# Performance work log

Hardware: AMD Instinct MI355X
Metric: run time of the kernel (lower is better)

Reference implementation:

```python
import jax, jax.numpy as jnp
import numpy as np

NEG_INF = -1e15  # matches masked_fill value -1000000000000000.0
ALPHA = 0.2      # leakyReLU negative slope


def setup_inputs() -> dict:
    key = jax.random.key(0)
    k1, k2, k3, k4 = jax.random.split(key, 4)
    N, F_IN, F_OUT = 8192, 256, 64
    x = jax.random.normal(k1, (N, F_IN), dtype=jnp.float32)
    mask = jax.random.randint(k2, (N, N), 0, 2, dtype=jnp.int32)
    trans = jax.random.normal(k3, (F_IN, F_OUT), dtype=jnp.float32) * 0.1
    attn = jax.random.normal(k4, (2 * F_OUT, 1), dtype=jnp.float32) * 0.1
    return {"x": x, "mask": mask, "trans": trans, "attn": attn}


def reference(x, mask, trans, attn):
    d = trans.shape[1]
    h = x @ trans                                  # [N, d]
    e1 = h @ attn[:d, :]                           # [N, 1]
    e2 = h @ attn[d:, :]                           # [N, 1]
    scores = jax.nn.leaky_relu(e1 + e2.T, negative_slope=ALPHA)  # [N, N]
    masked = jnp.where(mask == 0, NEG_INF, scores)
    attention = jax.nn.softmax(masked, axis=1)
    return attention @ h                           # [N, d]
```

## Files before the change

### kernel.cpp

```cpp
#include <hip/hip_runtime.h>
#include <hip/hip_bf16.h>
#include <math.h>

#define N 8192
#define FIN 256
#define D 64
#define ALPHA 0.2f

typedef __attribute__((ext_vector_type(8))) short bf16x8;
typedef __attribute__((ext_vector_type(4))) float f32x4;

__global__ __launch_bounds__(256) void k_h_e(
    const float* __restrict__ x, const float* __restrict__ trans,
    const float* __restrict__ attn,
    __hip_bfloat16* __restrict__ hF, float* __restrict__ e1, float* __restrict__ e2)
{
    __shared__ float xs[8 * FIN];
    __shared__ __hip_bfloat16 hl[8 * D];
    const int t = threadIdx.x;
    const int r0 = blockIdx.x * 8;

    #pragma unroll
    for (int v = 0; v < 2; ++v) {
        int idx = t + 256 * v;
        ((float4*)xs)[idx] = ((const float4*)(x + (size_t)r0 * FIN))[idx];
    }
    __syncthreads();

    const int lane = t & 63, w = t >> 6;
    const float* xa = xs + (2 * w) * FIN;
    const float* xb = xs + (2 * w + 1) * FIN;
    float acca = 0.f, accb = 0.f;
    #pragma unroll 8
    for (int k = 0; k < FIN; ++k) {
        const float tv = trans[k * D + lane];
        acca = fmaf(xa[k], tv, acca);
        accb = fmaf(xb[k], tv, accb);
    }
    const int ra = r0 + 2 * w, rb = ra + 1;

    const float a1 = attn[lane], a2 = attn[D + lane];
    float p1a = acca * a1, p2a = acca * a2;
    float p1b = accb * a1, p2b = accb * a2;
    #pragma unroll
    for (int mm = 1; mm <= 32; mm <<= 1) {
        p1a += __shfl_xor(p1a, mm);
        p2a += __shfl_xor(p2a, mm);
        p1b += __shfl_xor(p1b, mm);
        p2b += __shfl_xor(p2b, mm);
    }
    if (lane == 0) { e1[ra] = p1a; e2[ra] = p2a; e1[rb] = p1b; e2[rb] = p2b; }

    hl[(2 * w) * D + lane]     = __float2bfloat16(acca);
    hl[(2 * w + 1) * D + lane] = __float2bfloat16(accb);
    __syncthreads();
    if (t < D) {
        const int q = t >> 4, m = t & 15;
        const int cb = r0 >> 5, jgrp = (r0 >> 3) & 3;
        union { bf16x8 v; __hip_bfloat16 h[8]; } o;
        #pragma unroll
        for (int r = 0; r < 8; ++r) o.h[r] = hl[r * D + q * 16 + m];
        *(bf16x8*)(hF + (((size_t)cb * 4 + q) * 64 + jgrp * 16 + m) * 8) = o.v;
    }
}

__global__ __launch_bounds__(256) void k_attn(
    const int* __restrict__ mask, const __hip_bfloat16* __restrict__ hF,
    const float* __restrict__ e1, const float* __restrict__ e2,
    float* __restrict__ acc_part, float* __restrict__ l_part, int cs)
{
    const int t = threadIdx.x;
    const int lane = t & 63, wave = t >> 6;
    const int i0 = (blockIdx.y * 4 + wave) * 16;
    const int sp = blockIdx.x;
    const int c0 = sp * cs;
    const int m = lane & 15, quad = lane >> 4;
    const int row = i0 + m;
    const float er = e1[row];
    const size_t mrow = (size_t)row * N;

    const __hip_bfloat16* hfp = hF + (((size_t)(c0 >> 5)) * 4 * 64 + lane) * 8;

    f32x4 acc0 = {0.f, 0.f, 0.f, 0.f};
    f32x4 acc1 = {0.f, 0.f, 0.f, 0.f};
    f32x4 acc2 = {0.f, 0.f, 0.f, 0.f};
    f32x4 acc3 = {0.f, 0.f, 0.f, 0.f};
    float lsum = 0.f;

    const int iters = cs >> 5;
    #pragma unroll 2
    for (int it = 0; it < iters; ++it) {
        const int jb = c0 + it * 32 + quad * 8;
        const int4   m0 = *(const int4*)(mask + mrow + jb);
        const int4   m1 = *(const int4*)(mask + mrow + jb + 4);
        const float4 ea = *(const float4*)(e2 + jb);
        const float4 eb = *(const float4*)(e2 + jb + 4);
        const bf16x8* hq = (const bf16x8*)(hfp + (size_t)it * 2048);
        const bf16x8 b0 = hq[0];
        const bf16x8 b1 = hq[64];
        const bf16x8 b2 = hq[128];
        const bf16x8 b3 = hq[192];

        float s0 = er + ea.x; s0 = s0 > 0.f ? s0 : ALPHA * s0;
        float s1 = er + ea.y; s1 = s1 > 0.f ? s1 : ALPHA * s1;
        float s2 = er + ea.z; s2 = s2 > 0.f ? s2 : ALPHA * s2;
        float s3 = er + ea.w; s3 = s3 > 0.f ? s3 : ALPHA * s3;
        float s4 = er + eb.x; s4 = s4 > 0.f ? s4 : ALPHA * s4;
        float s5 = er + eb.y; s5 = s5 > 0.f ? s5 : ALPHA * s5;
        float s6 = er + eb.z; s6 = s6 > 0.f ? s6 : ALPHA * s6;
        float s7 = er + eb.w; s7 = s7 > 0.f ? s7 : ALPHA * s7;
        const float p0 = m0.x ? __expf(s0) : 0.f;
        const float p1 = m0.y ? __expf(s1) : 0.f;
        const float p2 = m0.z ? __expf(s2) : 0.f;
        const float p3 = m0.w ? __expf(s3) : 0.f;
        const float p4 = m1.x ? __expf(s4) : 0.f;
        const float p5 = m1.y ? __expf(s5) : 0.f;
        const float p6 = m1.z ? __expf(s6) : 0.f;
        const float p7 = m1.w ? __expf(s7) : 0.f;

        union { bf16x8 v; __hip_bfloat162 h2[4]; } af;
        af.h2[0] = __float22bfloat162_rn(make_float2(p0, p1));
        af.h2[1] = __float22bfloat162_rn(make_float2(p2, p3));
        af.h2[2] = __float22bfloat162_rn(make_float2(p4, p5));
        af.h2[3] = __float22bfloat162_rn(make_float2(p6, p7));

        lsum += ((p0 + p1) + (p2 + p3)) + ((p4 + p5) + (p6 + p7));

        acc0 = __builtin_amdgcn_mfma_f32_16x16x32_bf16(af.v, b0, acc0, 0, 0, 0);
        acc1 = __builtin_amdgcn_mfma_f32_16x16x32_bf16(af.v, b1, acc1, 0, 0, 0);
        acc2 = __builtin_amdgcn_mfma_f32_16x16x32_bf16(af.v, b2, acc2, 0, 0, 0);
        acc3 = __builtin_amdgcn_mfma_f32_16x16x32_bf16(af.v, b3, acc3, 0, 0, 0);
    }

    lsum += __shfl_xor(lsum, 16);
    lsum += __shfl_xor(lsum, 32);
    if (quad == 0) l_part[(size_t)sp * N + row] = lsum;

    #pragma unroll
    for (int reg = 0; reg < 4; ++reg) {
        const size_t rbase = ((size_t)sp * N + i0 + quad * 4 + reg) * D;
        acc_part[rbase + m     ] = acc0[reg];
        acc_part[rbase + m + 16] = acc1[reg];
        acc_part[rbase + m + 32] = acc2[reg];
        acc_part[rbase + m + 48] = acc3[reg];
    }
}

__global__ __launch_bounds__(256) void k_reduce(
    const float* __restrict__ acc_part, const float* __restrict__ l_part,
    float* __restrict__ out, int nsplit)
{
    const int idx = blockIdx.x * 256 + threadIdx.x;
    const int row = idx >> 6;
    float sum = 0.f, l = 0.f;
    for (int s = 0; s < nsplit; ++s) {
        sum += acc_part[(size_t)s * N * D + idx];
        l   += l_part[(size_t)s * N + row];
    }
    out[idx] = sum / l;
}

extern "C" void kernel_launch(void* const* d_in, const int* in_sizes, int n_in,
                              void* d_out, int out_size, void* d_ws, size_t ws_size,
                              hipStream_t stream) {
    const float* x     = (const float*)d_in[0];
    const int*   mask  = (const int*)d_in[1];
    const float* trans = (const float*)d_in[2];
    const float* attn  = (const float*)d_in[3];
    float* out = (float*)d_out;

    char* ws = (char*)d_ws;
    __hip_bfloat16* hF = (__hip_bfloat16*)ws;
    char* p = ws + (size_t)D * N * sizeof(__hip_bfloat16);
    float* e1 = (float*)p;            p += (size_t)N * sizeof(float);
    float* e2 = (float*)p;            p += (size_t)N * sizeof(float);

    const size_t used = (size_t)(p - ws);
    int nsplit = 4;
    while (nsplit > 1) {
        size_t need = used + (size_t)nsplit * N * sizeof(float)
                    + (size_t)nsplit * N * D * sizeof(float);
        if (need <= ws_size) break;
        nsplit >>= 1;
    }
    float* l_part = (float*)p;
    float* acc_part = l_part + (size_t)nsplit * N;

    k_h_e<<<N / 8, 256, 0, stream>>>(x, trans, attn, hF, e1, e2);
    dim3 g2(nsplit, N / 64);
    k_attn<<<g2, 256, 0, stream>>>(mask, hF, e1, e2, acc_part, l_part, N / nsplit);
    k_reduce<<<(N * D) / 256, 256, 0, stream>>>(acc_part, l_part, out, nsplit);
}
```

Measured before the change: 427.9 us.

## Stage mask rows into LDS via coalesced global_load_lds and prefetch h/e2 operands

The attention kernel now copies each wave's 16 mask rows, 256 columns at a time, into a padded per-wave LDS buffer using async global_load_lds. Each lane issues fully coalesced 16-byte loads instead of strided per-row loads. The h fragments and e2 values are software-prefetched one step ahead within each 256-column chunk. The intent is better DRAM efficiency on the 256MB mask stream. The cost is about 66KB of LDS per block, which may reduce occupancy, and a full vmcnt wait that serializes load and compute per chunk.

```diff
diff --git a/kernel.cpp b/kernel.cpp
--- a/kernel.cpp
+++ b/kernel.cpp
@@ -6,6 +6,8 @@
 #define FIN 256
 #define D 64
 #define ALPHA 0.2f
+#define SROW 1040
+#define WBUF (16 * SROW)
 
 typedef __attribute__((ext_vector_type(8))) short bf16x8;
 typedef __attribute__((ext_vector_type(4))) float f32x4;
@@ -69,6 +71,7 @@
     const float* __restrict__ e1, const float* __restrict__ e2,
     float* __restrict__ acc_part, float* __restrict__ l_part, int cs)
 {
+    __shared__ __align__(16) char smem[4 * WBUF];
     const int t = threadIdx.x;
     const int lane = t & 63, wave = t >> 6;
     const int i0 = (blockIdx.y * 4 + wave) * 16;
@@ -77,8 +80,9 @@
     const int m = lane & 15, quad = lane >> 4;
     const int row = i0 + m;
     const float er = e1[row];
-    const size_t mrow = (size_t)row * N;
-
+
+    char* sw = smem + wave * WBUF;
+    const char* swm = sw + m * SROW;
     const __hip_bfloat16* hfp = hF + (((size_t)(c0 >> 5)) * 4 * 64 + lane) * 8;
 
     f32x4 acc0 = {0.f, 0.f, 0.f, 0.f};
@@ -87,49 +91,79 @@
     f32x4 acc3 = {0.f, 0.f, 0.f, 0.f};
     float lsum = 0.f;
 
-    const int iters = cs >> 5;
-    #pragma unroll 2
-    for (int it = 0; it < iters; ++it) {
-        const int jb = c0 + it * 32 + quad * 8;
-        const int4   m0 = *(const int4*)(mask + mrow + jb);
-        const int4   m1 = *(const int4*)(mask + mrow + jb + 4);
-        const float4 ea = *(const float4*)(e2 + jb);
-        const float4 eb = *(const float4*)(e2 + jb + 4);
-        const bf16x8* hq = (const bf16x8*)(hfp + (size_t)it * 2048);
-        const bf16x8 b0 = hq[0];
-        const bf16x8 b1 = hq[64];
-        const bf16x8 b2 = hq[128];
-        const bf16x8 b3 = hq[192];
-
-        float s0 = er + ea.x; s0 = s0 > 0.f ? s0 : ALPHA * s0;
-        float s1 = er + ea.y; s1 = s1 > 0.f ? s1 : ALPHA * s1;
-        float s2 = er + ea.z; s2 = s2 > 0.f ? s2 : ALPHA * s2;
-        float s3 = er + ea.w; s3 = s3 > 0.f ? s3 : ALPHA * s3;
-        float s4 = er + eb.x; s4 = s4 > 0.f ? s4 : ALPHA * s4;
-        float s5 = er + eb.y; s5 = s5 > 0.f ? s5 : ALPHA * s5;
-        float s6 = er + eb.z; s6 = s6 > 0.f ? s6 : ALPHA * s6;
-        float s7 = er + eb.w; s7 = s7 > 0.f ? s7 : ALPHA * s7;
-        const float p0 = m0.x ? __expf(s0) : 0.f;
-        const float p1 = m0.y ? __expf(s1) : 0.f;
-        const float p2 = m0.z ? __expf(s2) : 0.f;
-        const float p3 = m0.w ? __expf(s3) : 0.f;
-        const float p4 = m1.x ? __expf(s4) : 0.f;
-        const float p5 = m1.y ? __expf(s5) : 0.f;
-        const float p6 = m1.z ? __expf(s6) : 0.f;
-        const float p7 = m1.w ? __expf(s7) : 0.f;
-
-        union { bf16x8 v; __hip_bfloat162 h2[4]; } af;
-        af.h2[0] = __float22bfloat162_rn(make_float2(p0, p1));
-        af.h2[1] = __float22bfloat162_rn(make_float2(p2, p3));
-        af.h2[2] = __float22bfloat162_rn(make_float2(p4, p5));
-        af.h2[3] = __float22bfloat162_rn(make_float2(p6, p7));
-
-        lsum += ((p0 + p1) + (p2 + p3)) + ((p4 + p5) + (p6 + p7));
-
-        acc0 = __builtin_amdgcn_mfma_f32_16x16x32_bf16(af.v, b0, acc0, 0, 0, 0);
-        acc1 = __builtin_amdgcn_mfma_f32_16x16x32_bf16(af.v, b1, acc1, 0, 0, 0);
-        acc2 = __builtin_amdgcn_mfma_f32_16x16x32_bf16(af.v, b2, acc2, 0, 0, 0);
-        acc3 = __builtin_amdgcn_mfma_f32_16x16x32_bf16(af.v, b3, acc3, 0, 0, 0);
+    const int nss = cs >> 8;
+
+    for (int ss = 0; ss < nss; ++ss) {
+        const int cb0 = c0 + ss * 256;
+        #pragma unroll
+        for (int r = 0; r < 16; ++r) {
+            const int* g = mask + (size_t)(i0 + r) * N + cb0 + lane * 4;
+            char* l = sw + r * SROW + lane * 16;
+            __builtin_amdgcn_global_load_lds(
+                (const __attribute__((address_space(1))) void*)g,
+                (__attribute__((address_space(3))) void*)l, 16, 0, 0);
+        }
+        __builtin_amdgcn_s_waitcnt(0x0F70);
+
+        const int itg0 = ss * 8;
+        bf16x8 pb0, pb1, pb2, pb3; float4 pea, peb;
+        {
+            const size_t ito = (size_t)itg0 * 2048;
+            pb0 = *(const bf16x8*)(hfp + ito);
+            pb1 = *(const bf16x8*)(hfp + ito + 512);
+            pb2 = *(const bf16x8*)(hfp + ito + 1024);
+            pb3 = *(const bf16x8*)(hfp + ito + 1536);
+            const int jb = cb0 + quad * 8;
+            pea = *(const float4*)(e2 + jb);
+            peb = *(const float4*)(e2 + jb + 4);
+        }
+        #pragma unroll
+        for (int p = 0; p < 8; ++p) {
+            const bf16x8 b0 = pb0, b1 = pb1, b2 = pb2, b3 = pb3;
+            const float4 ea = pea, eb = peb;
+            if (p < 7) {
+                const size_t ito = (size_t)(itg0 + p + 1) * 2048;
+                pb0 = *(const bf16x8*)(hfp + ito);
+                pb1 = *(const bf16x8*)(hfp + ito + 512);
+                pb2 = *(const bf16x8*)(hfp + ito + 1024);
+                pb3 = *(const bf16x8*)(hfp + ito + 1536);
+                const int jb = cb0 + (p + 1) * 32 + quad * 8;
+                pea = *(const float4*)(e2 + jb);
+                peb = *(const float4*)(e2 + jb + 4);
+            }
+            const int4 m0 = *(const int4*)(swm + p * 128 + quad * 32);
+            const int4 m1 = *(const int4*)(swm + p * 128 + quad * 32 + 16);
+
+            float s0 = er + ea.x; s0 = s0 > 0.f ? s0 : ALPHA * s0;
+            float s1 = er + ea.y; s1 = s1 > 0.f ? s1 : ALPHA * s1;
+            float s2 = er + ea.z; s2 = s2 > 0.f ? s2 : ALPHA * s2;
+            float s3 = er + ea.w; s3 = s3 > 0.f ? s3 : ALPHA * s3;
+            float s4 = er + eb.x; s4 = s4 > 0.f ? s4 : ALPHA * s4;
+            float s5 = er + eb.y; s5 = s5 > 0.f ? s5 : ALPHA * s5;
+            float s6 = er + eb.z; s6 = s6 > 0.f ? s6 : ALPHA * s6;
+            float s7 = er + eb.w; s7 = s7 > 0.f ? s7 : ALPHA * s7;
+            const float p0 = m0.x ? __expf(s0) : 0.f;
+            const float p1 = m0.y ? __expf(s1) : 0.f;
+            const float p2 = m0.z ? __expf(s2) : 0.f;
+            const float p3 = m0.w ? __expf(s3) : 0.f;
+            const float p4 = m1.x ? __expf(s4) : 0.f;
+            const float p5 = m1.y ? __expf(s5) : 0.f;
+            const float p6 = m1.z ? __expf(s6) : 0.f;
+            const float p7 = m1.w ? __expf(s7) : 0.f;
+
+            union { bf16x8 v; __hip_bfloat162 h2[4]; } af;
+            af.h2[0] = __float22bfloat162_rn(make_float2(p0, p1));
+            af.h2[1] = __float22bfloat162_rn(make_float2(p2, p3));
+            af.h2[2] = __float22bfloat162_rn(make_float2(p4, p5));
+            af.h2[3] = __float22bfloat162_rn(make_float2(p6, p7));
+
+            lsum += ((p0 + p1) + (p2 + p3)) + ((p4 + p5) + (p6 + p7));
+
+            acc0 = __builtin_amdgcn_mfma_f32_16x16x32_bf16(af.v, b0, acc0, 0, 0, 0);
+            acc1 = __builtin_amdgcn_mfma_f32_16x16x32_bf16(af.v, b1, acc1, 0, 0, 0);
+            acc2 = __builtin_amdgcn_mfma_f32_16x16x32_bf16(af.v, b2, acc2, 0, 0, 0);
+            acc3 = __builtin_amdgcn_mfma_f32_16x16x32_bf16(af.v, b3, acc3, 0, 0, 0);
+        }
     }
 
     lsum += __shfl_xor(lsum, 16);
```

Result: faster. 391.9 us (-8.4%).

## Double-buffer mask tiles into LDS via global_load_lds and prefetch h fragments

Applied to the files above, without the earlier changes.

Rewrites the attention kernel's main loop as a software pipeline. Each wave stages 16x128 mask tiles into padded LDS buffers with asynchronous global_load_lds and register-prefetches the next stage's bf16 h fragments while computing the current stage. The e2 slice is staged once into shared memory. The split count is fixed at 8 with 1024-column chunks, and launch bounds now request 2 blocks per CU. This is meant to hide the latency of the 256MB mask stream, at the cost of a large LDS footprint, many extra registers for the prefetched fragments, more partial sums for the reduce pass, and hand-coded waitcnt values that may be fragile.

```diff
diff --git a/kernel.cpp b/kernel.cpp
--- a/kernel.cpp
+++ b/kernel.cpp
@@ -6,6 +6,11 @@
 #define FIN 256
 #define D 64
 #define ALPHA 0.2f
+#define NSPLIT 8
+#define CS 1024
+#define NSS 8
+#define SROW 528
+#define WBUF (16 * SROW)
 
 typedef __attribute__((ext_vector_type(8))) short bf16x8;
 typedef __attribute__((ext_vector_type(4))) float f32x4;
@@ -64,21 +69,92 @@
     }
 }
 
-__global__ __launch_bounds__(256) void k_attn(
+
+#define GLDS(G, L, SZ) __builtin_amdgcn_global_load_lds( \
+    (const __attribute__((address_space(1))) void*)(G),  \
+    (__attribute__((address_space(3))) void*)(L), (SZ), 0, 0)
+
+#define STAGE_MASK(SSV, BUF)                                           \
+    {                                                                  \
+        const int cb_ = c0 + (SSV) * 128;                              \
+        _Pragma("unroll")                                              \
+        for (int r_ = 0; r_ < 16; ++r_) {                              \
+            const int* g_ = mask + (size_t)(i0 + r_) * N + cb_ + lane; \
+            char* l_ = (BUF) + r_ * SROW + lane * 4;                   \
+            GLDS(g_, l_, 4);                                           \
+            GLDS(g_ + 64, l_ + 256, 4);                                \
+        }                                                              \
+    }
+
+#define HOIST_HF(SSV, HX)                                              \
+    {                                                                  \
+        _Pragma("unroll")                                              \
+        for (int p_ = 0; p_ < 4; ++p_) {                               \
+            const size_t ito_ = (size_t)((SSV) * 4 + p_) * 2048;       \
+            HX[4 * p_ + 0] = *(const bf16x8*)(hfp + ito_);             \
+            HX[4 * p_ + 1] = *(const bf16x8*)(hfp + ito_ + 512);       \
+            HX[4 * p_ + 2] = *(const bf16x8*)(hfp + ito_ + 1024);      \
+            HX[4 * p_ + 3] = *(const bf16x8*)(hfp + ito_ + 1536);      \
+        }                                                              \
+    }
+
+#define COMPUTE_SS(SSV, BUF, HX)                                               \
+    {                                                                          \
+        const char* swm_ = (BUF) + m * SROW;                                   \
+        _Pragma("unroll")                                                      \
+        for (int p_ = 0; p_ < 4; ++p_) {                                       \
+            const int4 m0 = *(const int4*)(swm_ + p_ * 128 + quad * 32);       \
+            const int4 m1 = *(const int4*)(swm_ + p_ * 128 + quad * 32 + 16);  \
+            const int ec_ = (SSV) * 128 + p_ * 32 + quad * 8;                  \
+            const float4 ea = *(const float4*)(se2 + ec_);                     \
+            const float4 eb = *(const float4*)(se2 + ec_ + 4);                 \
+            float s0 = er + ea.x; s0 = s0 > 0.f ? s0 : ALPHA * s0;             \
+            float s1 = er + ea.y; s1 = s1 > 0.f ? s1 : ALPHA * s1;             \
+            float s2 = er + ea.z; s2 = s2 > 0.f ? s2 : ALPHA * s2;             \
+            float s3 = er + ea.w; s3 = s3 > 0.f ? s3 : ALPHA * s3;             \
+            float s4 = er + eb.x; s4 = s4 > 0.f ? s4 : ALPHA * s4;             \
+            float s5 = er + eb.y; s5 = s5 > 0.f ? s5 : ALPHA * s5;             \
+            float s6 = er + eb.z; s6 = s6 > 0.f ? s6 : ALPHA * s6;             \
+            float s7 = er + eb.w; s7 = s7 > 0.f ? s7 : ALPHA * s7;             \
+            const float p0 = m0.x ? __expf(s0) : 0.f;                          \
+            const float p1 = m0.y ? __expf(s1) : 0.f;                          \
+            const float p2 = m0.z ? __expf(s2) : 0.f;                          \
+            const float p3 = m0.w ? __expf(s3) : 0.f;                          \
+            const float p4 = m1.x ? __expf(s4) : 0.f;                          \
+            const float p5 = m1.y ? __expf(s5) : 0.f;                          \
+            const float p6 = m1.z ? __expf(s6) : 0.f;                          \
+            const float p7 = m1.w ? __expf(s7) : 0.f;                          \
+            union { bf16x8 v; __hip_bfloat162 h2[4]; } af;                     \
+            af.h2[0] = __float22bfloat162_rn(make_float2(p0, p1));             \
+            af.h2[1] = __float22bfloat162_rn(make_float2(p2, p3));             \
+            af.h2[2] = __float22bfloat162_rn(make_float2(p4, p5));             \
+            af.h2[3] = __float22bfloat162_rn(make_float2(p6, p7));             \
+            lsum += ((p0 + p1) + (p2 + p3)) + ((p4 + p5) + (p6 + p7));         \
+            acc0 = __builtin_amdgcn_mfma_f32_16x16x32_bf16(af.v, HX[4*p_+0], acc0, 0, 0, 0); \
+            acc1 = __builtin_amdgcn_mfma_f32_16x16x32_bf16(af.v, HX[4*p_+1], acc1, 0, 0, 0); \
+            acc2 = __builtin_amdgcn_mfma_f32_16x16x32_bf16(af.v, HX[4*p_+2], acc2, 0, 0, 0); \
+            acc3 = __builtin_amdgcn_mfma_f32_16x16x32_bf16(af.v, HX[4*p_+3], acc3, 0, 0, 0); \
+        }                                                                      \
+    }
+
+__global__ __launch_bounds__(256, 2) void k_attn(
     const int* __restrict__ mask, const __hip_bfloat16* __restrict__ hF,
     const float* __restrict__ e1, const float* __restrict__ e2,
-    float* __restrict__ acc_part, float* __restrict__ l_part, int cs)
+    float* __restrict__ acc_part, float* __restrict__ l_part)
 {
+    __shared__ __align__(16) char smask[8 * WBUF];
+    __shared__ __align__(16) float se2[CS];
     const int t = threadIdx.x;
     const int lane = t & 63, wave = t >> 6;
     const int i0 = (blockIdx.y * 4 + wave) * 16;
     const int sp = blockIdx.x;
-    const int c0 = sp * cs;
+    const int c0 = sp * CS;
     const int m = lane & 15, quad = lane >> 4;
     const int row = i0 + m;
     const float er = e1[row];
-    const size_t mrow = (size_t)row * N;
-
+
+    char* bufA = smask + (wave * 2 + 0) * WBUF;
+    char* bufB = smask + (wave * 2 + 1) * WBUF;
     const __hip_bfloat16* hfp = hF + (((size_t)(c0 >> 5)) * 4 * 64 + lane) * 8;
 
     f32x4 acc0 = {0.f, 0.f, 0.f, 0.f};
@@ -86,51 +162,31 @@
     f32x4 acc2 = {0.f, 0.f, 0.f, 0.f};
     f32x4 acc3 = {0.f, 0.f, 0.f, 0.f};
     float lsum = 0.f;
-
-    const int iters = cs >> 5;
-    #pragma unroll 2
-    for (int it = 0; it < iters; ++it) {
-        const int jb = c0 + it * 32 + quad * 8;
-        const int4   m0 = *(const int4*)(mask + mrow + jb);
-        const int4   m1 = *(const int4*)(mask + mrow + jb + 4);
-        const float4 ea = *(const float4*)(e2 + jb);
-        const float4 eb = *(const float4*)(e2 + jb + 4);
-        const bf16x8* hq = (const bf16x8*)(hfp + (size_t)it * 2048);
-        const bf16x8 b0 = hq[0];
-        const bf16x8 b1 = hq[64];
-        const bf16x8 b2 = hq[128];
-        const bf16x8 b3 = hq[192];
-
-        float s0 = er + ea.x; s0 = s0 > 0.f ? s0 : ALPHA * s0;
-        float s1 = er + ea.y; s1 = s1 > 0.f ? s1 : ALPHA * s1;
-        float s2 = er + ea.z; s2 = s2 > 0.f ? s2 : ALPHA * s2;
-        float s3 = er + ea.w; s3 = s3 > 0.f ? s3 : ALPHA * s3;
-        float s4 = er + eb.x; s4 = s4 > 0.f ? s4 : ALPHA * s4;
-        float s5 = er + eb.y; s5 = s5 > 0.f ? s5 : ALPHA * s5;
-        float s6 = er + eb.z; s6 = s6 > 0.f ? s6 : ALPHA * s6;
-        float s7 = er + eb.w; s7 = s7 > 0.f ? s7 : ALPHA * s7;
-        const float p0 = m0.x ? __expf(s0) : 0.f;
-        const float p1 = m0.y ? __expf(s1) : 0.f;
-        const float p2 = m0.z ? __expf(s2) : 0.f;
-        const float p3 = m0.w ? __expf(s3) : 0.f;
-        const float p4 = m1.x ? __expf(s4) : 0.f;
-        const float p5 = m1.y ? __expf(s5) : 0.f;
-        const float p6 = m1.z ? __expf(s6) : 0.f;
-        const float p7 = m1.w ? __expf(s7) : 0.f;
-
-        union { bf16x8 v; __hip_bfloat162 h2[4]; } af;
-        af.h2[0] = __float22bfloat162_rn(make_float2(p0, p1));
-        af.h2[1] = __float22bfloat162_rn(make_float2(p2, p3));
-        af.h2[2] = __float22bfloat162_rn(make_float2(p4, p5));
-        af.h2[3] = __float22bfloat162_rn(make_float2(p6, p7));
-
-        lsum += ((p0 + p1) + (p2 + p3)) + ((p4 + p5) + (p6 + p7));
-
-        acc0 = __builtin_amdgcn_mfma_f32_16x16x32_bf16(af.v, b0, acc0, 0, 0, 0);
-        acc1 = __builtin_amdgcn_mfma_f32_16x16x32_bf16(af.v, b1, acc1, 0, 0, 0);
-        acc2 = __builtin_amdgcn_mfma_f32_16x16x32_bf16(af.v, b2, acc2, 0, 0, 0);
-        acc3 = __builtin_amdgcn_mfma_f32_16x16x32_bf16(af.v, b3, acc3, 0, 0, 0);
-    }
+    bf16x8 hA[16], hB[16];
+
+    if (wave == 0) {
+        #pragma unroll
+        for (int i = 0; i < 16; ++i)
+            GLDS(e2 + c0 + i * 64 + lane, (char*)se2 + i * 256 + lane * 4, 4);
+    }
+    STAGE_MASK(0, bufA);
+    HOIST_HF(0, hA);
+    __syncthreads();
+
+    for (int s2 = 0; s2 < NSS; s2 += 2) {
+        __builtin_amdgcn_s_waitcnt(0x4F70);
+        STAGE_MASK(s2 + 1, bufB);
+        HOIST_HF(s2 + 1, hB);
+        COMPUTE_SS(s2, bufA, hA);
+        __builtin_amdgcn_s_waitcnt(0x4F70);
+        {
+            const int sn = (s2 + 2 < NSS) ? s2 + 2 : s2 + 1;
+            STAGE_MASK(sn, bufA);
+            HOIST_HF(sn, hA);
+        }
+        COMPUTE_SS(s2 + 1, bufB, hB);
+    }
+    __builtin_amdgcn_s_waitcnt(0x0F70);
 
     lsum += __shfl_xor(lsum, 16);
     lsum += __shfl_xor(lsum, 32);
@@ -174,20 +230,11 @@
     char* p = ws + (size_t)D * N * sizeof(__hip_bfloat16);
     float* e1 = (float*)p;            p += (size_t)N * sizeof(float);
     float* e2 = (float*)p;            p += (size_t)N * sizeof(float);
-
-    const size_t used = (size_t)(p - ws);
-    int nsplit = 4;
-    while (nsplit > 1) {
-        size_t need = used + (size_t)nsplit * N * sizeof(float)
-                    + (size_t)nsplit * N * D * sizeof(float);
-        if (need <= ws_size) break;
-        nsplit >>= 1;
-    }
-    float* l_part = (float*)p;
-    float* acc_part = l_part + (size_t)nsplit * N;
+    float* l_part = (float*)p;        p += (size_t)NSPLIT * N * sizeof(float);
+    float* acc_part = (float*)p;
 
     k_h_e<<<N / 8, 256, 0, stream>>>(x, trans, attn, hF, e1, e2);
-    dim3 g2(nsplit, N / 64);
-    k_attn<<<g2, 256, 0, stream>>>(mask, hF, e1, e2, acc_part, l_part, N / nsplit);
-    k_reduce<<<(N * D) / 256, 256, 0, stream>>>(acc_part, l_part, out, nsplit);
-}
+    dim3 g2(NSPLIT, N / 64);
+    k_attn<<<g2, 256, 0, stream>>>(mask, hF, e1, e2, acc_part, l_part);
+    k_reduce<<<(N * D) / 256, 256, 0, stream>>>(acc_part, l_part, out, NSPLIT);
+}
```

New measurement: 401.4 us. 1.07x faster.
